# Optimization experiments

Measured on AMD Instinct MI355X. Metric: run time of the kernel, lower is better.

The kernel has to match this reference:

```python
import jax, jax.numpy as jnp
import numpy as np

B, S, D, M = 4, 2048, 1024, 4  # batch, seq_len, d_model, n_stride_masks


def setup_inputs() -> dict:
    key = jax.random.key(0)
    ks = jax.random.split(key, 10)
    lin = lambda k: jax.random.normal(k, (D, D), jnp.float32) / np.float32(np.sqrt(D))
    return {
        "x": jax.random.normal(ks[0], (B, S, D), jnp.float32),
        "stride_masks": jax.random.randint(ks[1], (M, S, S), 0, 2, jnp.int32),
        "Wq": lin(ks[2]), "bq": jnp.zeros((D,), jnp.float32),
        "Wk": lin(ks[3]), "bk": jnp.zeros((D,), jnp.float32),
        "Wv": lin(ks[4]), "bv": jnp.zeros((D,), jnp.float32),
        "Wo": lin(ks[5]), "bo": jnp.zeros((D,), jnp.float32),
    }


def reference(x, stride_masks, Wq, bq, Wk, bk, Wv, bv, Wo, bo):
    scale = jnp.float32(np.sqrt(D))
    Q = x @ Wq + bq  # [B,S,D]
    K = x @ Wk + bk
    V = x @ Wv + bv
    # scores are identical for every mask; compute once (same math as the loop)
    scores = jnp.einsum("bqd,bkd->bqk", Q, K) / scale  # [B,S,S]
    masked = jnp.where(stride_masks[:, None] == 0, jnp.float32(-1e9), scores[None])  # [M,B,S,S]
    weights = jax.nn.softmax(masked, axis=-1)
    # sum over masks then divide by M == mean(stack(outs), 0)
    out = jnp.einsum("mbqk,bkd->bqd", weights, V) / jnp.float32(M)
    return out @ Wo + bo
```

## Files before the change

### kernel.cpp

```cpp
#include <hip/hip_runtime.h>
#include <hip/hip_bf16.h>
#include <stdint.h>

#define B_ 4
#define S_ 2048
#define D_ 1024
#define M_ 4

typedef __bf16 bf16;
typedef _Float16 f16;
typedef unsigned char u8;
typedef __bf16 bf16x8 __attribute__((ext_vector_type(8)));
typedef _Float16 f16x8 __attribute__((ext_vector_type(8)));
typedef float f32x4 __attribute__((ext_vector_type(4)));

__device__ __forceinline__ void async_copy16(const void* g, void* l) {
  __builtin_amdgcn_global_load_lds(
      (const __attribute__((address_space(1))) void*)g,
      (__attribute__((address_space(3))) void*)l, 16, 0, 0);
}

__global__ __launch_bounds__(256) void prep(
    const float* __restrict__ x, const float* __restrict__ w0,
    const float* __restrict__ w1, const float* __restrict__ w2,
    const float* __restrict__ w3, const int* __restrict__ masks,
    bf16* __restrict__ xc, bf16* __restrict__ WT, u8* __restrict__ pk) {
  __shared__ bf16 t[64][65];
  const int blk = blockIdx.x;
  const int tid = threadIdx.x;
  const long SS = (long)S_ * S_;

  if (blk < 4096) {
    const long i = (long)blk * 2048 + tid * 8;
    const float4 a = *(const float4*)(x + i);
    const float4 b = *(const float4*)(x + i + 4);
    bf16x8 o;
    o[0] = (bf16)a.x; o[1] = (bf16)a.y; o[2] = (bf16)a.z; o[3] = (bf16)a.w;
    o[4] = (bf16)b.x; o[5] = (bf16)b.y; o[6] = (bf16)b.z; o[7] = (bf16)b.w;
    *(bf16x8*)(xc + i) = o;
  } else if (blk < 5120) {
    const int local = blk - 4096;
    const int z = local >> 8;
    const int rem = local & 255;
    const int r0 = (rem >> 4) * 64;
    const int c0 = (rem & 15) * 64;
    const int tx = tid & 63;
    const int ty = tid >> 6;
    const float* in = (z == 0) ? w0 : (z == 1) ? w1 : (z == 2) ? w2 : w3;
    bf16* out = WT + (long)z * D_ * D_;
    for (int i = ty; i < 64; i += 4)
      t[i][tx] = (bf16)in[(long)(r0 + i) * D_ + c0 + tx];
    __syncthreads();
    for (int i = ty; i < 64; i += 4)
      out[(long)(c0 + i) * D_ + r0 + tx] = t[tx][i];
  } else {
    const long e = (long)(blk - 5120) * 2048 + tid * 8;
    unsigned long long wv = 0;
#pragma unroll
    for (int m = 0; m < M_; ++m) {
      const int4 a = *(const int4*)(masks + m * SS + e);
      const int4 b = *(const int4*)(masks + m * SS + e + 4);
      const int v[8] = {a.x, a.y, a.z, a.w, b.x, b.y, b.z, b.w};
#pragma unroll
      for (int j = 0; j < 8; ++j)
        wv |= (unsigned long long)(v[j] != 0 ? 1u : 0u) << (8 * j + m);
    }
    *(unsigned long long*)(pk + e) = wv;
  }
}

__global__ __launch_bounds__(256) void transposeB(
    const bf16* __restrict__ in, bf16* __restrict__ out,
    int rows, int cols, long ib, long ob) {
  __shared__ bf16 t[64][65];
  in += (long)blockIdx.z * ib;
  out += (long)blockIdx.z * ob;
  const int r0 = blockIdx.y * 64;
  const int c0 = blockIdx.x * 64;
  const int tx = threadIdx.x & 63;
  const int ty = threadIdx.x >> 6;
#pragma unroll
  for (int i = ty; i < 64; i += 4) t[i][tx] = in[(long)(r0 + i) * cols + c0 + tx];
  __syncthreads();
#pragma unroll
  for (int i = ty; i < 64; i += 4) out[(long)(c0 + i) * rows + r0 + tx] = t[tx][i];
}

#define MODE_PLAIN 0
#define MODE_EXP 1
#define MODE_QKV 2
#define MODE_PV 3

template <typename OutT, int MODE>
__global__ __launch_bounds__(512) void gemmA(
    const bf16* __restrict__ A, int lda,
    const bf16* __restrict__ Bt, long bzs, int ldb,
    OutT* __restrict__ C, int ldc,
    const float* __restrict__ bias0, const float* __restrict__ bias1,
    const float* __restrict__ bias2, float alpha, int K) {
  __shared__ __align__(16) bf16 As[3][256 * 32];
  __shared__ __align__(16) bf16 Bs[3][128 * 32];
  const int tid = threadIdx.x;
  const int lane = tid & 63;
  const int w = tid >> 6;
  const int wm = w & 3;
  const int wn = w >> 2;
  const int quad = lane >> 4;
  const int l15 = lane & 15;
  const int fse = (quad ^ ((l15 >> 1) & 3)) << 3;

  const int gx = gridDim.x;
  const int pid = blockIdx.y * gx + blockIdx.x;
  const int gsz = 8 * gx;
  const int bym = (pid / gsz) * 8 + (pid % 8);
  const int bxm = (pid % gsz) / 8;
  const int row0 = bym * 256;
  const int col0 = bxm * 128;

  const bf16* Arow = A + (long)row0 * lda;
  const bf16* Bcol;
  int grp = 0;
  if (MODE == MODE_QKV) {
    grp = col0 >> 10;
    Bcol = Bt + (long)grp * ((long)D_ * D_) + (long)(col0 & (D_ - 1)) * ldb;
  } else if (MODE == MODE_PV || MODE == MODE_EXP) {
    Bcol = Bt + (long)(row0 >> 11) * bzs + (long)col0 * ldb;
  } else {
    Bcol = Bt + (long)col0 * ldb;
  }

  const int sr = tid >> 2;
  const int sc = ((tid & 3) ^ ((tid >> 3) & 3)) << 3;
  const bf16* gA = Arow + (long)sr * lda + sc;
  const bf16* gB = Bcol + (long)sr * ldb + sc;
  const int dstoff = (tid >> 6) << 9;
  const long a128 = (long)128 * lda;

#define STAGE(h, s)                                                    \
  {                                                                    \
    const int kc_ = (h) * 32;                                          \
    bf16* da_ = &As[0][0] + (s) * (256 * 32) + dstoff;                 \
    bf16* db_ = &Bs[0][0] + (s) * (128 * 32) + dstoff;                 \
    async_copy16(gA + kc_, da_);                                       \
    async_copy16(gA + kc_ + a128, da_ + 4096);                         \
    async_copy16(gB + kc_, db_);                                       \
  }

#define READF(Ra, Rb, s)                                                   \
  {                                                                        \
    const bf16* pa_ = &As[0][0] + (s) * (256 * 32);                        \
    const bf16* pb_ = &Bs[0][0] + (s) * (128 * 32);                        \
    _Pragma("unroll") for (int j = 0; j < 4; ++j) {                        \
      Ra[j] = *(const bf16x8*)&pa_[(wm * 64 + j * 16 + l15) * 32 + fse];   \
      Rb[j] = *(const bf16x8*)&pb_[(wn * 64 + j * 16 + l15) * 32 + fse];   \
    }                                                                      \
  }

#define MM(Ra, Rb)                                                         \
  __builtin_amdgcn_s_setprio(1);                                           \
  _Pragma("unroll") for (int mi = 0; mi < 4; ++mi)                         \
      _Pragma("unroll") for (int ni = 0; ni < 4; ++ni) acc[mi][ni] =       \
          __builtin_amdgcn_mfma_f32_16x16x32_bf16(Ra[mi], Rb[ni],          \
                                                  acc[mi][ni], 0, 0, 0);   \
  __builtin_amdgcn_s_setprio(0);

  f32x4 acc[4][4];
#pragma unroll
  for (int i = 0; i < 4; ++i)
#pragma unroll
    for (int j = 0; j < 4; ++j) acc[i][j] = (f32x4){0.f, 0.f, 0.f, 0.f};

  const int nh = (K >> 6) << 1;

  STAGE(0, 0);
  STAGE(1, 1);
  asm volatile("s_waitcnt vmcnt(3)" ::: "memory");
  __builtin_amdgcn_s_barrier();
  __builtin_amdgcn_sched_barrier(0);

  int s0 = 0;
  for (int h = 0; h < nh; ++h) {
    bf16x8 af[4], bf[4];
    READF(af, bf, s0);
    if (h + 2 < nh) {
      const int s2 = (s0 >= 1) ? (s0 - 1) : 2;
      STAGE(h + 2, s2);
    }
    MM(af, bf);
    if (h + 2 < nh)
      asm volatile("s_waitcnt vmcnt(3)" ::: "memory");
    else if (h + 1 < nh)
      asm volatile("s_waitcnt vmcnt(0)" ::: "memory");
    if (h + 1 < nh) {
      __builtin_amdgcn_s_barrier();
      __builtin_amdgcn_sched_barrier(0);
    }
    s0 = (s0 == 2) ? 0 : (s0 + 1);
  }

#undef STAGE
#undef READF
#undef MM

  const float* bias = (MODE == MODE_QKV)
                          ? (grp == 0 ? bias0 : grp == 1 ? bias1 : bias2)
                          : bias0;
  const long NX = (long)B_ * S_ * D_;
  OutT* Cb = (MODE == MODE_QKV) ? C + (long)grp * NX : C;
#pragma unroll
  for (int mi = 0; mi < 4; ++mi)
#pragma unroll
    for (int ni = 0; ni < 4; ++ni) {
      const int col = col0 + wn * 64 + ni * 16 + l15;
      const int ccol = (MODE == MODE_QKV) ? (col & (D_ - 1)) : col;
      const float bv = bias ? bias[ccol] : 0.0f;
#pragma unroll
      for (int r = 0; r < 4; ++r) {
        const int row = row0 + wm * 64 + mi * 16 + quad * 4 + r;
        const float val = acc[mi][ni][r] * alpha + bv;
        if (MODE == MODE_EXP) {
          Cb[(long)row * ldc + col] = (OutT)__expf(val);
        } else if (MODE == MODE_QKV) {
          Cb[(long)row * D_ + ccol] = (OutT)val;
        } else {
          Cb[(long)row * ldc + col] = (OutT)val;
        }
      }
    }
}

template <typename OutT, int MODE>
__global__ __launch_bounds__(256) void gemmB(
    const bf16* __restrict__ A, int lda,
    const bf16* __restrict__ Bt, long bzs, int ldb,
    OutT* __restrict__ C, int ldc,
    const float* __restrict__ bias0, const float* __restrict__ bias1,
    const float* __restrict__ bias2, float alpha, int K) {
  __shared__ __align__(16) bf16 As[3][256 * 32];
  __shared__ __align__(16) bf16 Bs[3][128 * 32];
  const int tid = threadIdx.x;
  const int lane = tid & 63;
  const int w = tid >> 6;
  const int wm = w & 1;
  const int wn = w >> 1;
  const int quad = lane >> 4;
  const int l15 = lane & 15;
  const int fse = (quad ^ ((l15 >> 1) & 3)) << 3;

  const int gx = gridDim.x;
  const int pid = blockIdx.y * gx + blockIdx.x;
  const int gsz = 8 * gx;
  const int bym = (pid / gsz) * 8 + (pid % 8);
  const int bxm = (pid % gsz) / 8;
  const int row0 = bym * 256;
  const int col0 = bxm * 128;

  const bf16* Arow = A + (long)row0 * lda;
  const bf16* Bcol;
  int grp = 0;
  if (MODE == MODE_QKV) {
    grp = col0 >> 10;
    Bcol = Bt + (long)grp * ((long)D_ * D_) + (long)(col0 & (D_ - 1)) * ldb;
  } else if (MODE == MODE_PV || MODE == MODE_EXP) {
    Bcol = Bt + (long)(row0 >> 11) * bzs + (long)col0 * ldb;
  } else {
    Bcol = Bt + (long)col0 * ldb;
  }

  const int sr = tid >> 2;
  const int sc = ((tid & 3) ^ ((tid >> 3) & 3)) << 3;
  const bf16* gA = Arow + (long)sr * lda + sc;
  const bf16* gB = Bcol + (long)sr * ldb + sc;
  const int dstoff = (tid >> 6) << 9;
  const long a64 = (long)64 * lda;
  const long b64 = (long)64 * ldb;

#define STAGE(h, s)                                                    \
  {                                                                    \
    const int kc_ = (h) * 32;                                          \
    bf16* da_ = &As[0][0] + (s) * (256 * 32) + dstoff;                 \
    bf16* db_ = &Bs[0][0] + (s) * (128 * 32) + dstoff;                 \
    async_copy16(gA + kc_, da_);                                       \
    async_copy16(gA + kc_ + a64, da_ + 2048);                          \
    async_copy16(gA + kc_ + 2 * a64, da_ + 4096);                      \
    async_copy16(gA + kc_ + 3 * a64, da_ + 6144);                      \
    async_copy16(gB + kc_, db_);                                       \
    async_copy16(gB + kc_ + b64, db_ + 2048);                          \
  }

#define READF(Ra, Rb, s)                                                    \
  {                                                                         \
    const bf16* pa_ = &As[0][0] + (s) * (256 * 32);                         \
    const bf16* pb_ = &Bs[0][0] + (s) * (128 * 32);                         \
    _Pragma("unroll") for (int j = 0; j < 8; ++j)                           \
        Ra[j] = *(const bf16x8*)&pa_[(wm * 128 + j * 16 + l15) * 32 + fse]; \
    _Pragma("unroll") for (int j = 0; j < 4; ++j)                           \
        Rb[j] = *(const bf16x8*)&pb_[(wn * 64 + j * 16 + l15) * 32 + fse];  \
  }

#define MM(Ra, Rb)                                                         \
  __builtin_amdgcn_s_setprio(1);                                           \
  _Pragma("unroll") for (int mi = 0; mi < 8; ++mi)                         \
      _Pragma("unroll") for (int ni = 0; ni < 4; ++ni) acc[mi][ni] =       \
          __builtin_amdgcn_mfma_f32_16x16x32_bf16(Ra[mi], Rb[ni],          \
                                                  acc[mi][ni], 0, 0, 0);   \
  __builtin_amdgcn_s_setprio(0);

  f32x4 acc[8][4];
#pragma unroll
  for (int i = 0; i < 8; ++i)
#pragma unroll
    for (int j = 0; j < 4; ++j) acc[i][j] = (f32x4){0.f, 0.f, 0.f, 0.f};

  const int nh = (K >> 6) << 1;

  STAGE(0, 0);
  STAGE(1, 1);
  asm volatile("s_waitcnt vmcnt(6)" ::: "memory");
  __builtin_amdgcn_s_barrier();
  __builtin_amdgcn_sched_barrier(0);

  int s0 = 0;
  for (int h = 0; h < nh; ++h) {
    bf16x8 af[8], bf[4];
    READF(af, bf, s0);
    if (h + 2 < nh) {
      const int s2 = (s0 >= 1) ? (s0 - 1) : 2;
      STAGE(h + 2, s2);
    }
    MM(af, bf);
    if (h + 2 < nh)
      asm volatile("s_waitcnt vmcnt(6)" ::: "memory");
    else if (h + 1 < nh)
      asm volatile("s_waitcnt vmcnt(0)" ::: "memory");
    if (h + 1 < nh) {
      __builtin_amdgcn_s_barrier();
      __builtin_amdgcn_sched_barrier(0);
    }
    s0 = (s0 == 2) ? 0 : (s0 + 1);
  }

#undef STAGE
#undef READF
#undef MM

  const float* bias = (MODE == MODE_QKV)
                          ? (grp == 0 ? bias0 : grp == 1 ? bias1 : bias2)
                          : bias0;
  const long NX = (long)B_ * S_ * D_;
  OutT* Cb = (MODE == MODE_QKV) ? C + (long)grp * NX : C;
#pragma unroll
  for (int mi = 0; mi < 8; ++mi)
#pragma unroll
    for (int ni = 0; ni < 4; ++ni) {
      const int col = col0 + wn * 64 + ni * 16 + l15;
      const int ccol = (MODE == MODE_QKV) ? (col & (D_ - 1)) : col;
      const float bv = bias ? bias[ccol] : 0.0f;
#pragma unroll
      for (int r = 0; r < 4; ++r) {
        const int row = row0 + wm * 128 + mi * 16 + quad * 4 + r;
        const float val = acc[mi][ni][r] * alpha + bv;
        if (MODE == MODE_EXP) {
          Cb[(long)row * ldc + col] = (OutT)__expf(val);
        } else if (MODE == MODE_QKV) {
          Cb[(long)row * D_ + ccol] = (OutT)val;
        } else {
          Cb[(long)row * ldc + col] = (OutT)val;
        }
      }
    }
}

__global__ __launch_bounds__(256) void softmax_combine(
    const f16* __restrict__ E, const u8* __restrict__ pk, bf16* __restrict__ P) {
  const int q = blockIdx.x;
  const int b = blockIdx.y;
  const int tid = threadIdx.x;
  const int lane = tid & 63;
  const int wv = tid >> 6;
  __shared__ float4 red[4];

  float e[8];
  {
    const f16x8 h = *(const f16x8*)(E + ((long)b * S_ + q) * S_ + tid * 8);
#pragma unroll
    for (int j = 0; j < 8; ++j) e[j] = (float)h[j];
  }
  const unsigned long long mb =
      *(const unsigned long long*)(pk + (long)q * S_ + tid * 8);

  float4 s = {0.f, 0.f, 0.f, 0.f};
#pragma unroll
  for (int j = 0; j < 8; ++j) {
    const unsigned bits = (unsigned)(mb >> (8 * j)) & 0xF;
    const float ev = e[j];
    if (bits & 1) s.x += ev;
    if (bits & 2) s.y += ev;
    if (bits & 4) s.z += ev;
    if (bits & 8) s.w += ev;
  }
#pragma unroll
  for (int o = 32; o > 0; o >>= 1) {
    s.x += __shfl_xor(s.x, o, 64);
    s.y += __shfl_xor(s.y, o, 64);
    s.z += __shfl_xor(s.z, o, 64);
    s.w += __shfl_xor(s.w, o, 64);
  }
  if (lane == 0) red[wv] = s;
  __syncthreads();
  const float4 t0 = red[0], t1 = red[1], t2 = red[2], t3 = red[3];
  const float r0 = 0.25f / (t0.x + t1.x + t2.x + t3.x);
  const float r1 = 0.25f / (t0.y + t1.y + t2.y + t3.y);
  const float r2 = 0.25f / (t0.z + t1.z + t2.z + t3.z);
  const float r3 = 0.25f / (t0.w + t1.w + t2.w + t3.w);

  bf16x8 o;
#pragma unroll
  for (int j = 0; j < 8; ++j) {
    const unsigned bits = (unsigned)(mb >> (8 * j)) & 0xF;
    const float wgt = ((bits & 1) ? r0 : 0.f) + ((bits & 2) ? r1 : 0.f) +
                      ((bits & 4) ? r2 : 0.f) + ((bits & 8) ? r3 : 0.f);
    o[j] = (bf16)(e[j] * wgt);
  }
  *(bf16x8*)(P + ((long)b * S_ + q) * S_ + tid * 8) = o;
}

extern "C" void kernel_launch(void* const* d_in, const int* in_sizes, int n_in,
                              void* d_out, int out_size, void* d_ws, size_t ws_size,
                              hipStream_t stream) {
  const float* x = (const float*)d_in[0];
  const int* masks = (const int*)d_in[1];
  const float* bq = (const float*)d_in[3];
  const float* bk = (const float*)d_in[5];
  const float* bv = (const float*)d_in[7];
  const float* bo = (const float*)d_in[9];
  float* out = (float*)d_out;

  const long DD = (long)D_ * D_;
  const long SD = (long)S_ * D_;
  const long NX = (long)B_ * SD;
  const long SS = (long)S_ * S_;

  bf16* xc = (bf16*)d_ws;
  bf16* WqT = xc + NX;
  bf16* WoT = WqT + 3 * DD;
  u8* pk = (u8*)(WoT + DD);
  bf16* Q = (bf16*)(pk + SS);
  bf16* K = Q + NX;
  bf16* V = K + NX;
  bf16* VT = V + NX;
  bf16* P = VT + NX;
  f16* E = (f16*)(P + (long)B_ * SS);
  bf16* attn = Q;

  dim3 blk(256);
  dim3 blk512(512);

  prep<<<dim3(7168), blk, 0, stream>>>(
      x, (const float*)d_in[2], (const float*)d_in[4], (const float*)d_in[6],
      (const float*)d_in[8], masks, xc, WqT, pk);

  gemmB<bf16, MODE_QKV><<<dim3(24, 32), blk, 0, stream>>>(
      xc, D_, WqT, 0, D_, Q, D_, bq, bk, bv, 1.0f, D_);

  transposeB<<<dim3(16, 32, B_), blk, 0, stream>>>(V, VT, S_, D_, SD, SD);

  gemmB<f16, MODE_EXP><<<dim3(16, 32), blk, 0, stream>>>(
      Q, D_, K, SD, D_, E, S_, nullptr, nullptr, nullptr, 1.0f / 32.0f, D_);

  softmax_combine<<<dim3(S_, B_), blk, 0, stream>>>(E, pk, P);

  gemmA<bf16, MODE_PV><<<dim3(8, 32), blk512, 0, stream>>>(
      P, S_, VT, SD, S_, attn, D_, nullptr, nullptr, nullptr, 1.0f, S_);

  gemmA<float, MODE_PLAIN><<<dim3(8, 32), blk512, 0, stream>>>(
      attn, D_, WoT, 0, D_, out, D_, bo, nullptr, nullptr, 1.0f, D_);
}
```

Before: 393.4 us.

## Swap GEMM kernel variants: gemmA for QKV/scores, new 256x64 gemmC for PV/out

Replaces the 256-thread 256x128-tile gemmB with a new 512-thread gemmC using 256x64 tiles, where only half the warps stage B. gemmC is used for the PV and output projections, doubling their grid to 16x32 blocks. The QKV and score GEMMs move to the existing 512-thread gemmA at their previous grid sizes. The intent is more blocks and waves in flight for the smaller GEMMs, at the cost of less reuse per tile.

After: 357.7 us. 9.1% less time.

```diff
diff --git a/kernel.cpp b/kernel.cpp
--- a/kernel.cpp
+++ b/kernel.cpp
@@ -230,19 +230,18 @@
 }
 
 template <typename OutT, int MODE>
-__global__ __launch_bounds__(256) void gemmB(
+__global__ __launch_bounds__(512) void gemmC(
     const bf16* __restrict__ A, int lda,
     const bf16* __restrict__ Bt, long bzs, int ldb,
     OutT* __restrict__ C, int ldc,
-    const float* __restrict__ bias0, const float* __restrict__ bias1,
-    const float* __restrict__ bias2, float alpha, int K) {
+    const float* __restrict__ bias0, float alpha, int K) {
   __shared__ __align__(16) bf16 As[3][256 * 32];
-  __shared__ __align__(16) bf16 Bs[3][128 * 32];
+  __shared__ __align__(16) bf16 Bs[3][64 * 32];
   const int tid = threadIdx.x;
   const int lane = tid & 63;
   const int w = tid >> 6;
-  const int wm = w & 1;
-  const int wn = w >> 1;
+  const int wm = w & 3;
+  const int wn = w >> 2;
   const int quad = lane >> 4;
   const int l15 = lane & 15;
   const int fse = (quad ^ ((l15 >> 1) & 3)) << 3;
@@ -253,86 +252,85 @@
   const int bym = (pid / gsz) * 8 + (pid % 8);
   const int bxm = (pid % gsz) / 8;
   const int row0 = bym * 256;
-  const int col0 = bxm * 128;
+  const int col0 = bxm * 64;
 
   const bf16* Arow = A + (long)row0 * lda;
-  const bf16* Bcol;
-  int grp = 0;
-  if (MODE == MODE_QKV) {
-    grp = col0 >> 10;
-    Bcol = Bt + (long)grp * ((long)D_ * D_) + (long)(col0 & (D_ - 1)) * ldb;
-  } else if (MODE == MODE_PV || MODE == MODE_EXP) {
-    Bcol = Bt + (long)(row0 >> 11) * bzs + (long)col0 * ldb;
-  } else {
-    Bcol = Bt + (long)col0 * ldb;
-  }
+  const bf16* Bcol = (MODE == MODE_PV)
+                         ? Bt + (long)(row0 >> 11) * bzs + (long)col0 * ldb
+                         : Bt + (long)col0 * ldb;
 
   const int sr = tid >> 2;
   const int sc = ((tid & 3) ^ ((tid >> 3) & 3)) << 3;
   const bf16* gA = Arow + (long)sr * lda + sc;
   const bf16* gB = Bcol + (long)sr * ldb + sc;
   const int dstoff = (tid >> 6) << 9;
-  const long a64 = (long)64 * lda;
-  const long b64 = (long)64 * ldb;
+  const long a128 = (long)128 * lda;
+  const bool bstage = (w < 4);
 
 #define STAGE(h, s)                                                    \
   {                                                                    \
     const int kc_ = (h) * 32;                                          \
     bf16* da_ = &As[0][0] + (s) * (256 * 32) + dstoff;                 \
-    bf16* db_ = &Bs[0][0] + (s) * (128 * 32) + dstoff;                 \
     async_copy16(gA + kc_, da_);                                       \
-    async_copy16(gA + kc_ + a64, da_ + 2048);                          \
-    async_copy16(gA + kc_ + 2 * a64, da_ + 4096);                      \
-    async_copy16(gA + kc_ + 3 * a64, da_ + 6144);                      \
-    async_copy16(gB + kc_, db_);                                       \
-    async_copy16(gB + kc_ + b64, db_ + 2048);                          \
-  }
-
-#define READF(Ra, Rb, s)                                                    \
-  {                                                                         \
-    const bf16* pa_ = &As[0][0] + (s) * (256 * 32);                         \
-    const bf16* pb_ = &Bs[0][0] + (s) * (128 * 32);                         \
-    _Pragma("unroll") for (int j = 0; j < 8; ++j)                           \
-        Ra[j] = *(const bf16x8*)&pa_[(wm * 128 + j * 16 + l15) * 32 + fse]; \
-    _Pragma("unroll") for (int j = 0; j < 4; ++j)                           \
-        Rb[j] = *(const bf16x8*)&pb_[(wn * 64 + j * 16 + l15) * 32 + fse];  \
+    async_copy16(gA + kc_ + a128, da_ + 4096);                         \
+    if (bstage) {                                                      \
+      bf16* db_ = &Bs[0][0] + (s) * (64 * 32) + dstoff;                \
+      async_copy16(gB + kc_, db_);                                     \
+    }                                                                  \
+  }
+
+#define VMW(n3, n2)                                                    \
+  if (bstage)                                                          \
+    asm volatile("s_waitcnt vmcnt(" #n3 ")" ::: "memory");             \
+  else                                                                 \
+    asm volatile("s_waitcnt vmcnt(" #n2 ")" ::: "memory");
+
+#define READF(Ra, Rb, s)                                                   \
+  {                                                                        \
+    const bf16* pa_ = &As[0][0] + (s) * (256 * 32);                        \
+    const bf16* pb_ = &Bs[0][0] + (s) * (64 * 32);                         \
+    _Pragma("unroll") for (int j = 0; j < 4; ++j)                          \
+        Ra[j] = *(const bf16x8*)&pa_[(wm * 64 + j * 16 + l15) * 32 + fse]; \
+    _Pragma("unroll") for (int j = 0; j < 2; ++j)                          \
+        Rb[j] = *(const bf16x8*)&pb_[(wn * 32 + j * 16 + l15) * 32 + fse]; \
   }
 
 #define MM(Ra, Rb)                                                         \
   __builtin_amdgcn_s_setprio(1);                                           \
-  _Pragma("unroll") for (int mi = 0; mi < 8; ++mi)                         \
-      _Pragma("unroll") for (int ni = 0; ni < 4; ++ni) acc[mi][ni] =       \
+  _Pragma("unroll") for (int mi = 0; mi < 4; ++mi)                         \
+      _Pragma("unroll") for (int ni = 0; ni < 2; ++ni) acc[mi][ni] =       \
           __builtin_amdgcn_mfma_f32_16x16x32_bf16(Ra[mi], Rb[ni],          \
                                                   acc[mi][ni], 0, 0, 0);   \
   __builtin_amdgcn_s_setprio(0);
 
-  f32x4 acc[8][4];
-#pragma unroll
-  for (int i = 0; i < 8; ++i)
-#pragma unroll
-    for (int j = 0; j < 4; ++j) acc[i][j] = (f32x4){0.f, 0.f, 0.f, 0.f};
+  f32x4 acc[4][2];
+#pragma unroll
+  for (int i = 0; i < 4; ++i)
+#pragma unroll
+    for (int j = 0; j < 2; ++j) acc[i][j] = (f32x4){0.f, 0.f, 0.f, 0.f};
 
   const int nh = (K >> 6) << 1;
 
   STAGE(0, 0);
   STAGE(1, 1);
-  asm volatile("s_waitcnt vmcnt(6)" ::: "memory");
+  VMW(3, 2);
   __builtin_amdgcn_s_barrier();
   __builtin_amdgcn_sched_barrier(0);
 
   int s0 = 0;
   for (int h = 0; h < nh; ++h) {
-    bf16x8 af[8], bf[4];
+    bf16x8 af[4], bf[2];
     READF(af, bf, s0);
     if (h + 2 < nh) {
       const int s2 = (s0 >= 1) ? (s0 - 1) : 2;
       STAGE(h + 2, s2);
     }
     MM(af, bf);
-    if (h + 2 < nh)
-      asm volatile("s_waitcnt vmcnt(6)" ::: "memory");
-    else if (h + 1 < nh)
+    if (h + 2 < nh) {
+      VMW(3, 2);
+    } else if (h + 1 < nh) {
       asm volatile("s_waitcnt vmcnt(0)" ::: "memory");
+    }
     if (h + 1 < nh) {
       __builtin_amdgcn_s_barrier();
       __builtin_amdgcn_sched_barrier(0);
@@ -341,32 +339,20 @@
   }
 
 #undef STAGE
+#undef VMW
 #undef READF
 #undef MM
 
-  const float* bias = (MODE == MODE_QKV)
-                          ? (grp == 0 ? bias0 : grp == 1 ? bias1 : bias2)
-                          : bias0;
-  const long NX = (long)B_ * S_ * D_;
-  OutT* Cb = (MODE == MODE_QKV) ? C + (long)grp * NX : C;
-#pragma unroll
-  for (int mi = 0; mi < 8; ++mi)
-#pragma unroll
-    for (int ni = 0; ni < 4; ++ni) {
-      const int col = col0 + wn * 64 + ni * 16 + l15;
-      const int ccol = (MODE == MODE_QKV) ? (col & (D_ - 1)) : col;
-      const float bv = bias ? bias[ccol] : 0.0f;
+#pragma unroll
+  for (int mi = 0; mi < 4; ++mi)
+#pragma unroll
+    for (int ni = 0; ni < 2; ++ni) {
+      const int col = col0 + wn * 32 + ni * 16 + l15;
+      const float bv = bias0 ? bias0[col] : 0.0f;
 #pragma unroll
       for (int r = 0; r < 4; ++r) {
-        const int row = row0 + wm * 128 + mi * 16 + quad * 4 + r;
-        const float val = acc[mi][ni][r] * alpha + bv;
-        if (MODE == MODE_EXP) {
-          Cb[(long)row * ldc + col] = (OutT)__expf(val);
-        } else if (MODE == MODE_QKV) {
-          Cb[(long)row * D_ + ccol] = (OutT)val;
-        } else {
-          Cb[(long)row * ldc + col] = (OutT)val;
-        }
+        const int row = row0 + wm * 64 + mi * 16 + quad * 4 + r;
+        C[(long)row * ldc + col] = (OutT)(acc[mi][ni][r] * alpha + bv);
       }
     }
 }
@@ -460,19 +446,19 @@
       x, (const float*)d_in[2], (const float*)d_in[4], (const float*)d_in[6],
       (const float*)d_in[8], masks, xc, WqT, pk);
 
-  gemmB<bf16, MODE_QKV><<<dim3(24, 32), blk, 0, stream>>>(
+  gemmA<bf16, MODE_QKV><<<dim3(24, 32), blk512, 0, stream>>>(
       xc, D_, WqT, 0, D_, Q, D_, bq, bk, bv, 1.0f, D_);
 
   transposeB<<<dim3(16, 32, B_), blk, 0, stream>>>(V, VT, S_, D_, SD, SD);
 
-  gemmB<f16, MODE_EXP><<<dim3(16, 32), blk, 0, stream>>>(
+  gemmA<f16, MODE_EXP><<<dim3(16, 32), blk512, 0, stream>>>(
       Q, D_, K, SD, D_, E, S_, nullptr, nullptr, nullptr, 1.0f / 32.0f, D_);
 
   softmax_combine<<<dim3(S_, B_), blk, 0, stream>>>(E, pk, P);
 
-  gemmA<bf16, MODE_PV><<<dim3(8, 32), blk512, 0, stream>>>(
-      P, S_, VT, SD, S_, attn, D_, nullptr, nullptr, nullptr, 1.0f, S_);
-
-  gemmA<float, MODE_PLAIN><<<dim3(8, 32), blk512, 0, stream>>>(
-      attn, D_, WoT, 0, D_, out, D_, bo, nullptr, nullptr, 1.0f, D_);
-}
+  gemmC<bf16, MODE_PV><<<dim3(16, 32), blk512, 0, stream>>>(
+      P, S_, VT, SD, S_, attn, D_, nullptr, 1.0f, S_);
+
+  gemmC<float, MODE_PLAIN><<<dim3(16, 32), blk512, 0, stream>>>(
+      attn, D_, WoT, 0, D_, out, D_, bo, 1.0f, D_);
+}
```
